# Kernel optimization log

Hardware: AMD Instinct MI355X
Metric: run time of the kernel (lower is better)

Reference implementation:

```python
import jax, jax.numpy as jnp
import numpy as np

B, Lq, D = 2, 4096, 768
NH, NP, NL = 6, 4, 1
Hs, Ws = 128, 128
Lf = Hs * Ws
DH = D // NH
EPS = 1e-6


def _ln(x, g, b):
    m = jnp.mean(x, -1, keepdims=True)
    v = jnp.mean(jnp.square(x - m), -1, keepdims=True)
    return (x - m) * jax.lax.rsqrt(v + EPS) * g + b


def setup_inputs() -> dict:
    key = jax.random.key(0)
    ks = jax.random.split(key, 20)
    s = 0.02
    rn = lambda k, shape, sc=s: (jax.random.normal(k, shape, jnp.float32) * sc)
    return {
        'query': jax.random.normal(ks[0], (B, Lq, D), jnp.float32),
        'reference_points': jax.random.uniform(ks[1], (B, Lq, NL, 2), jnp.float32),
        'feat': jax.random.normal(ks[2], (B, Lf, D), jnp.float32),
        'feat_other_modalities': jax.random.normal(ks[3], (B, Lq, D), jnp.float32),
        'spatial_shapes': jnp.array([[Hs, Ws]], jnp.int32),
        'level_start_index': jnp.array([0], jnp.int32),
        'qn_g': jnp.ones(D), 'qn_b': jnp.zeros(D),
        'fn_g': jnp.ones(D), 'fn_b': jnp.zeros(D),
        'W_off': rn(ks[4], (D, NH * NL * NP * 2)), 'b_off': jnp.zeros(NH * NL * NP * 2),
        'W_attn': rn(ks[5], (D, NH * NL * NP)), 'b_attn': jnp.zeros(NH * NL * NP),
        'W_val': rn(ks[6], (D, D)), 'b_val': jnp.zeros(D),
        'W_out': rn(ks[7], (D, D)), 'b_out': jnp.zeros(D),
        'gamma': rn(ks[8], (D,), 0.1),
        'qnm_g': jnp.ones(D), 'qnm_b': jnp.zeros(D),
        'fnm_g': jnp.ones(D), 'fnm_b': jnp.zeros(D),
        'ada_w0': rn(ks[9], (D, D // 4)), 'ada_b0': jnp.zeros(D // 4),
        'ada_w1': rn(ks[10], (D, D // 4)), 'ada_b1': jnp.zeros(D // 4),
        'ada_w2': rn(ks[11], (D // 4, D)), 'ada_b2': jnp.zeros(D),
        'gamma_om': rn(ks[12], (D,), 0.1),
    }


def _msdeform_attn(query_n, reference_points, feat_n, Hi, Wi,
                   W_off, b_off, W_attn, b_attn, W_val, b_val, W_out, b_out):
    Bv = query_n.shape[0]
    value = (feat_n @ W_val + b_val).reshape(Bv, Lf, NH, DH)
    value = value.transpose(0, 2, 1, 3)  # (B, NH, Lf, DH)

    off = (query_n @ W_off + b_off).reshape(Bv, Lq, NH, NL, NP, 2)
    aw = (query_n @ W_attn + b_attn).reshape(Bv, Lq, NH, NL * NP)
    aw = jax.nn.softmax(aw, axis=-1).reshape(Bv, Lq, NH, NL, NP)

    normalizer = jnp.array([Wi, Hi], jnp.float32)  # [W, H]
    loc = reference_points[:, :, None, :, None, :] + off / normalizer  # (B,Lq,NH,NL,NP,2)
    loc = loc[:, :, :, 0]  # single level -> (B, Lq, NH, NP, 2)

    # grid_sample align_corners=False, padding zeros
    x = loc[..., 0] * Wi - 0.5
    y = loc[..., 1] * Hi - 0.5
    x0 = jnp.floor(x); y0 = jnp.floor(y)
    wx1 = x - x0; wx0 = 1.0 - wx1
    wy1 = y - y0; wy0 = 1.0 - wy1
    x0i = x0.astype(jnp.int32); y0i = y0.astype(jnp.int32)
    x1i = x0i + 1; y1i = y0i + 1

    def t(a):  # (B,Lq,NH,NP) -> (B,NH,Lq,NP,1)
        return a.transpose(0, 2, 1, 3)[..., None]

    def gather(yy, xx):
        valid = (xx >= 0) & (xx < Wi) & (yy >= 0) & (yy < Hi)
        idx = jnp.clip(yy, 0, Hi - 1) * Wi + jnp.clip(xx, 0, Wi - 1)  # (B,Lq,NH,NP)
        idx = idx.transpose(0, 2, 1, 3).reshape(Bv, NH, Lq * NP)
        g = jnp.take_along_axis(value, idx[..., None], axis=2)  # (B,NH,Lq*NP,DH)
        g = g.reshape(Bv, NH, Lq, NP, DH)
        return g * t(valid.astype(jnp.float32))

    sampled = (gather(y0i, x0i) * t(wy0 * wx0) + gather(y0i, x1i) * t(wy0 * wx1)
               + gather(y1i, x0i) * t(wy1 * wx0) + gather(y1i, x1i) * t(wy1 * wx1))
    awT = aw[:, :, :, 0].transpose(0, 2, 1, 3)[..., None]  # (B,NH,Lq,NP,1)
    out = jnp.sum(sampled * awT, axis=3)  # (B,NH,Lq,DH)
    out = out.transpose(0, 2, 1, 3).reshape(Bv, Lq, D)
    return out @ W_out + b_out


def reference(query, reference_points, feat, feat_other_modalities, spatial_shapes,
              level_start_index, qn_g, qn_b, fn_g, fn_b, W_off, b_off, W_attn, b_attn,
              W_val, b_val, W_out, b_out, gamma, qnm_g, qnm_b, fnm_g, fnm_b,
              ada_w0, ada_b0, ada_w1, ada_b1, ada_w2, ada_b2, gamma_om):
    Hi = int(np.asarray(spatial_shapes)[0, 0]); Wi = int(np.asarray(spatial_shapes)[0, 1])
    query_n = _ln(query, qn_g, qn_b)
    feat_n = _ln(feat, fn_g, fn_b)
    attn = _msdeform_attn(query_n, reference_points, feat_n, Hi, Wi,
                          W_off, b_off, W_attn, b_attn, W_val, b_val, W_out, b_out)
    q = query + gamma * attn
    fom_n = _ln(feat_other_modalities, fnm_g, fnm_b)
    qn2 = _ln(q, qnm_g, qnm_b)
    p = qn2 @ ada_w0 + ada_b0
    xm = fom_n @ ada_w1 + ada_b1
    prompted = (p + xm) @ ada_w2 + ada_b2
    q = q + gamma_om * prompted
    return (q, prompted)
```

## Files before the change

### kernel.cpp

```cpp
#include <hip/hip_runtime.h>
#include <hip/hip_bf16.h>

typedef long long i64;

#define B_   2
#define LQ   4096
#define D_   768
#define NH_  6
#define NP_  4
#define DH_  128
#define LF   16384
#define NQ_ROWS (B_*LQ)
#define NF_ROWS (B_*LF)
#define QSIZE (NQ_ROWS*D_)

typedef __bf16 bf16x8 __attribute__((ext_vector_type(8)));
typedef float  f32x4  __attribute__((ext_vector_type(4)));

__device__ __forceinline__ float load_in(const void* p, i64 i, int bf) {
  if (bf) return __bfloat162float(((const __hip_bfloat16*)p)[i]);
  return ((const float*)p)[i];
}
__device__ __forceinline__ float us2f(unsigned short u) {
  unsigned v = (unsigned)u << 16;
  return __uint_as_float(v);
}
__device__ __forceinline__ unsigned short f2us(float f) {
  __hip_bfloat16 h = __float2bfloat16(f);
  return *(unsigned short*)&h;
}

__global__ void k_detect(const void* probe, int* flag) {
  unsigned v = *(const unsigned*)probe;
  *flag = (v == 0x3F803F80u) ? 1 : 0;
}

#define NCVT 18
struct CvtArgs { const void* src[NCVT]; float* dst[NCVT]; int n[NCVT]; };
__global__ void k_cvt(CvtArgs a, const int* flag) {
  int bf = *flag;
  int ai = blockIdx.y;
  int n = a.n[ai];
  const void* s = a.src[ai];
  float* d = a.dst[ai];
  for (int i = blockIdx.x * blockDim.x + threadIdx.x; i < n; i += gridDim.x * blockDim.x)
    d[i] = load_in(s, i, bf);
}

#define NTT 7
struct TtArgs {
  const void* src[NTT]; __hip_bfloat16* dst[NTT];
  int K[NTT]; int N[NTT]; int Nt[NTT];
  int tileBase[NTT]; int tilesN[NTT];
};
__global__ void k_transpose(TtArgs a, const int* flag) {
  __shared__ float lds[64][65];
  int bf = *flag;
  int t = blockIdx.x;
  int e = 0;
  #pragma unroll
  for (int i = 1; i < NTT; ++i) if (t >= a.tileBase[i]) e = i;
  int lt = t - a.tileBase[e];
  int tn = lt % a.tilesN[e], tk = lt / a.tilesN[e];
  int K = a.K[e], N = a.N[e], Nt = a.Nt[e];
  int k0 = tk * 64, n0 = tn * 64;
  int tid = threadIdx.x;
  int cl = tid & 63, rw = tid >> 6;
  const void* s = a.src[e];
  #pragma unroll
  for (int i = 0; i < 16; ++i) {
    int kl = rw * 16 + i;
    int n = n0 + cl;
    float v = (n < N) ? load_in(s, (i64)(k0 + kl) * N + n, bf) : 0.f;
    lds[kl][cl] = v;
  }
  __syncthreads();
  __hip_bfloat16* d = a.dst[e];
  #pragma unroll
  for (int i = 0; i < 16; ++i) {
    int nl = rw * 16 + i;
    int n = n0 + nl;
    if (n < Nt) d[(i64)n * K + k0 + cl] = __float2bfloat16(lds[cl][nl]);
  }
}

struct Ln3Args {
  const void* src0; const void* src1; const void* src2;
  const float *g0, *b0, *g1, *b1, *g2, *b2;
  __hip_bfloat16 *d0, *d1, *d2;
};
__device__ __forceinline__ void ln_row(const void* src, const float* g, const float* b,
                                       __hip_bfloat16* dst, int row, int lane, int bf) {
  float v[12];
  if (bf) {
    const ushort4* s = (const ushort4*)src + (i64)row * 192;
    #pragma unroll
    for (int j = 0; j < 3; ++j) {
      ushort4 u = s[lane + j * 64];
      v[j*4+0] = us2f(u.x); v[j*4+1] = us2f(u.y); v[j*4+2] = us2f(u.z); v[j*4+3] = us2f(u.w);
    }
  } else {
    const float4* s = (const float4*)src + (i64)row * 192;
    #pragma unroll
    for (int j = 0; j < 3; ++j) {
      float4 u = s[lane + j * 64];
      v[j*4+0] = u.x; v[j*4+1] = u.y; v[j*4+2] = u.z; v[j*4+3] = u.w;
    }
  }
  float s1 = 0.f, s2 = 0.f;
  #pragma unroll
  for (int i = 0; i < 12; ++i) { s1 += v[i]; s2 += v[i] * v[i]; }
  #pragma unroll
  for (int o = 32; o > 0; o >>= 1) { s1 += __shfl_xor(s1, o, 64); s2 += __shfl_xor(s2, o, 64); }
  float mean = s1 * (1.f / 768.f);
  float var = s2 * (1.f / 768.f) - mean * mean;
  float rstd = rsqrtf(var + 1e-6f);
  uint2* dv = (uint2*)dst + (i64)row * 192;
  #pragma unroll
  for (int j = 0; j < 3; ++j) {
    int gi = lane + j * 64;
    float4 gg = ((const float4*)g)[gi];
    float4 bb = ((const float4*)b)[gi];
    unsigned short u0 = f2us((v[j*4+0] - mean) * rstd * gg.x + bb.x);
    unsigned short u1 = f2us((v[j*4+1] - mean) * rstd * gg.y + bb.y);
    unsigned short u2 = f2us((v[j*4+2] - mean) * rstd * gg.z + bb.z);
    unsigned short u3 = f2us((v[j*4+3] - mean) * rstd * gg.w + bb.w);
    uint2 o;
    o.x = (unsigned)u0 | ((unsigned)u1 << 16);
    o.y = (unsigned)u2 | ((unsigned)u3 << 16);
    dv[gi] = o;
  }
}
__global__ void k_ln3(Ln3Args a, const int* flag) {
  int bf = *flag;
  int gw = blockIdx.x * 4 + (threadIdx.x >> 6);
  int lane = threadIdx.x & 63;
  if (gw < NF_ROWS)                 ln_row(a.src0, a.g0, a.b0, a.d0, gw,                   lane, bf);
  else if (gw < NF_ROWS + NQ_ROWS)  ln_row(a.src1, a.g1, a.b1, a.d1, gw - NF_ROWS,         lane, bf);
  else                              ln_row(a.src2, a.g2, a.b2, a.d2, gw - NF_ROWS - NQ_ROWS, lane, bf);
}
__global__ void k_ln_q(const float* src, const float* g, const float* b,
                       __hip_bfloat16* dst) {
  int gw = blockIdx.x * 4 + (threadIdx.x >> 6);
  int lane = threadIdx.x & 63;
  ln_row(src, g, b, dst, gw, lane, 0);
}

__device__ __forceinline__ void load_lds16(const void* g, void* l) {
  __builtin_amdgcn_global_load_lds((__attribute__((address_space(1))) void*)g,
                                   (__attribute__((address_space(3))) void*)l, 16, 0, 0);
}

template<int EPI>
__global__ void k_mgemm(const __hip_bfloat16* __restrict__ A, const __hip_bfloat16* __restrict__ Wt,
                        const float* __restrict__ bias, void* __restrict__ Cp,
                        int M, int N, int K, int Nx,
                        const void* aux0, const float* __restrict__ aux1, const int* flag) {
  __shared__ __align__(16) __hip_bfloat16 sm[2 * 8192];
  __hip_bfloat16* As = sm;
  __hip_bfloat16* Bs = sm + 8192;
  const int tid  = threadIdx.x;
  const int w    = tid >> 6, lane = tid & 63;
  const int quad = lane >> 4, l15 = lane & 15;
  const int f = blockIdx.x;
  const int xcd = f & 7, s8 = f >> 3;
  const int bn = (s8 % Nx) * 128;
  const int bm = (xcd + (s8 / Nx) * 8) * 128;
  const int wm = (w >> 1) * 64, wn = (w & 1) * 64;
  const int bfv = (EPI == 2 || EPI == 3) ? *flag : 0;

  int rowS[4], colS[4];
  #pragma unroll
  for (int j = 0; j < 4; ++j) {
    int p = j * 256 + tid;
    int r = p >> 3, pc = p & 7;
    rowS[j] = r; colS[j] = (pc ^ (r & 7)) * 8;
  }

  f32x4 acc[4][4];
  #pragma unroll
  for (int i = 0; i < 4; ++i)
    #pragma unroll
    for (int j = 0; j < 4; ++j) acc[i][j] = (f32x4){0.f, 0.f, 0.f, 0.f};

  const __hip_bfloat16* Ab = A  + (i64)bm * K;
  const __hip_bfloat16* Bb = Wt + (i64)bn * K;

  for (int k0 = 0; k0 < K; k0 += 64) {
    #pragma unroll
    for (int j = 0; j < 4; ++j) {
      load_lds16(Ab + (i64)rowS[j] * K + k0 + colS[j], As + (j * 256 + w * 64) * 8);
      load_lds16(Bb + (i64)rowS[j] * K + k0 + colS[j], Bs + (j * 256 + w * 64) * 8);
    }
    __syncthreads();
    bf16x8 af[2][4], bg[2][4];
    #pragma unroll
    for (int s = 0; s < 2; ++s) {
      #pragma unroll
      for (int i = 0; i < 4; ++i) {
        int ra = wm + i * 16 + l15;
        af[s][i] = *(const bf16x8*)(As + (ra * 8 + ((s * 4 + quad) ^ (ra & 7))) * 8);
        int rb = wn + i * 16 + l15;
        bg[s][i] = *(const bf16x8*)(Bs + (rb * 8 + ((s * 4 + quad) ^ (rb & 7))) * 8);
      }
    }
    #pragma unroll
    for (int s = 0; s < 2; ++s)
      #pragma unroll
      for (int i = 0; i < 4; ++i)
        #pragma unroll
        for (int j = 0; j < 4; ++j)
          acc[i][j] = __builtin_amdgcn_mfma_f32_16x16x32_bf16(af[s][i], bg[s][j], acc[i][j], 0, 0, 0);
    __syncthreads();
  }

  #pragma unroll
  for (int j = 0; j < 4; ++j) {
    int col = bn + wn + j * 16 + l15;
    if (col >= N) continue;
    float bv = bias[col];
    #pragma unroll
    for (int i = 0; i < 4; ++i) {
      #pragma unroll
      for (int r = 0; r < 4; ++r) {
        int row = bm + wm + i * 16 + quad * 4 + r;
        float v = acc[i][j][r] + bv;
        i64 idx = (i64)row * N + col;
        if (EPI == 0) {
          ((__hip_bfloat16*)Cp)[idx] = __float2bfloat16(v);
        } else if (EPI == 1) {
          ((float*)Cp)[idx] = v;
        } else if (EPI == 2) {
          ((float*)Cp)[idx] = load_in(aux0, idx, bfv) + aux1[col] * v;
        } else if (EPI == 4) {
          ((__hip_bfloat16*)Cp)[idx] = __float2bfloat16(((const float*)aux0)[idx] + v);
        } else {
          float qv = ((const float*)aux0)[idx] + aux1[col] * v;
          if (bfv) {
            ((__hip_bfloat16*)Cp)[idx]         = __float2bfloat16(qv);
            ((__hip_bfloat16*)Cp)[QSIZE + idx] = __float2bfloat16(v);
          } else {
            ((float*)Cp)[idx]         = qv;
            ((float*)Cp)[QSIZE + idx] = v;
          }
        }
      }
    }
  }
}

__global__ void k_sample(const __hip_bfloat16* __restrict__ val, const float* __restrict__ ref,
                         const float* __restrict__ oa, const int* __restrict__ ss,
                         __hip_bfloat16* __restrict__ out) {
  int gid = blockIdx.x * blockDim.x + threadIdx.x;
  int gw = gid >> 6, lane = gid & 63;
  if (gw >= B_*LQ*NH_) return;
  int h = gw % NH_;
  int bq = gw / NH_;
  int b = bq / LQ;
  int Hi = ss[0], Wi = ss[1];
  float Wf = (float)Wi, Hf = (float)Hi;
  const float* op = oa + (i64)bq*72 + h*8;
  const float* ap = oa + (i64)bq*72 + 48 + h*4;
  float rx = ref[(i64)bq*2], ry = ref[(i64)bq*2 + 1];
  float a0 = ap[0], a1 = ap[1], a2 = ap[2], a3 = ap[3];
  float mx = fmaxf(fmaxf(a0, a1), fmaxf(a2, a3));
  float e0 = expf(a0-mx), e1 = expf(a1-mx), e2 = expf(a2-mx), e3 = expf(a3-mx);
  float inv = 1.0f / (e0+e1+e2+e3);
  float wts[4] = {e0*inv, e1*inv, e2*inv, e3*inv};
  const __hip_bfloat16* vb = val + (i64)b*LF*D_ + h*DH_ + lane*2;
  float accx = 0.f, accy = 0.f;
  #pragma unroll
  for (int p = 0; p < NP_; ++p) {
    float x = rx*Wf + op[p*2+0] - 0.5f;
    float y = ry*Hf + op[p*2+1] - 0.5f;
    float xf = floorf(x), yf = floorf(y);
    int x0 = (int)xf, y0 = (int)yf;
    float wx1 = x - xf, wx0 = 1.f - wx1;
    float wy1 = y - yf, wy0 = 1.f - wy1;
    float aw = wts[p];
    #pragma unroll
    for (int c = 0; c < 4; ++c) {
      int xi = x0 + (c & 1), yi = y0 + (c >> 1);
      float wgt = aw * ((c & 1) ? wx1 : wx0) * ((c >> 1) ? wy1 : wy0);
      if (xi >= 0 && xi < Wi && yi >= 0 && yi < Hi && wgt != 0.f) {
        __hip_bfloat162 g = *(const __hip_bfloat162*)(vb + (i64)(yi*Wi + xi)*D_);
        accx += wgt * __bfloat162float(g.x); accy += wgt * __bfloat162float(g.y);
      }
    }
  }
  __hip_bfloat162 o2;
  o2.x = __float2bfloat16(accx); o2.y = __float2bfloat16(accy);
  *(__hip_bfloat162*)(out + (i64)bq*D_ + h*DH_ + lane*2) = o2;
}

extern "C" void kernel_launch(void* const* d_in, const int* in_sizes, int n_in,
                              void* d_out, int out_size, void* d_ws, size_t ws_size,
                              hipStream_t stream) {
  char* base = (char*)d_ws;
  size_t o = 0;
  auto alloc = [&](size_t bytes) { size_t r = o; o += (bytes + 63) & ~(size_t)63; return r; };
  auto F = [&](size_t off) { return (float*)(base + off); };
  auto H = [&](size_t off) { return (__hip_bfloat16*)(base + off); };

  size_t FLAG  = alloc(64);
  size_t REF   = alloc(NQ_ROWS*2*4);
  size_t QN_G  = alloc(768*4); size_t QN_B = alloc(768*4);
  size_t FN_G  = alloc(768*4); size_t FN_B = alloc(768*4);
  size_t BOA   = alloc(128*4);
  size_t BVAL  = alloc(768*4); size_t BOUT = alloc(768*4);
  size_t GAMMA = alloc(768*4);
  size_t QNM_G = alloc(768*4); size_t QNM_B = alloc(768*4);
  size_t FNM_G = alloc(768*4); size_t FNM_B = alloc(768*4);
  size_t AB0   = alloc(192*4); size_t AB1  = alloc(192*4);
  size_t AB2   = alloc(768*4); size_t GOM  = alloc(768*4);
  size_t WT_VAL = alloc((size_t)768*768*2);
  size_t WT_OUT = alloc((size_t)768*768*2);
  size_t WT_OA  = alloc((size_t)128*768*2);
  size_t WT_A0  = alloc((size_t)256*768*2);
  size_t WT_A1  = alloc((size_t)256*768*2);
  size_t WT_A2  = alloc((size_t)768*192*2);
  size_t FEATN  = alloc((size_t)NF_ROWS*768*2);
  size_t VALUE  = alloc((size_t)NF_ROWS*768*2);
  size_t QN     = alloc((size_t)NQ_ROWS*768*2);
  size_t FOMN   = alloc((size_t)NQ_ROWS*768*2);
  size_t ATTNP  = alloc((size_t)NQ_ROWS*768*2);
  size_t QN2    = alloc((size_t)NQ_ROWS*768*2);
  size_t PXM    = alloc((size_t)NQ_ROWS*192*2);
  size_t OA     = alloc((size_t)NQ_ROWS*72*4);
  size_t QBUF   = alloc((size_t)QSIZE*4);
  size_t PBUF   = alloc((size_t)NQ_ROWS*192*4);

  int* flag = (int*)(base + FLAG);

  k_detect<<<1, 1, 0, stream>>>(d_in[6], flag);

  {
    CvtArgs ca;
    const int   idx[NCVT]  = {1,6,7,8,9,11,13,15,17,18,19,20,21,22,24,26,28,29};
    const size_t dof[NCVT] = {REF,QN_G,QN_B,FN_G,FN_B,BOA,BOA+48*4,BVAL,BOUT,GAMMA,
                              QNM_G,QNM_B,FNM_G,FNM_B,AB0,AB1,AB2,GOM};
    for (int i = 0; i < NCVT; ++i) { ca.src[i] = d_in[idx[i]]; ca.dst[i] = F(dof[i]); ca.n[i] = in_sizes[idx[i]]; }
    k_cvt<<<dim3(8, NCVT), 256, 0, stream>>>(ca, flag);
  }
  {
    TtArgs ta;
    const int   src[NTT]  = {14, 16, 10, 12, 23, 25, 27};
    const size_t dst[NTT] = {WT_VAL, WT_OUT, WT_OA, WT_OA + (size_t)48*768*2, WT_A0, WT_A1, WT_A2};
    const int Kk[NTT] = {768, 768, 768, 768, 768, 768, 192};
    const int Nn[NTT] = {768, 768,  48,  24, 192, 192, 768};
    const int Nt[NTT] = {768, 768,  48,  80, 256, 256, 768};
    int tb = 0;
    for (int i = 0; i < NTT; ++i) {
      ta.src[i] = d_in[src[i]]; ta.dst[i] = H(dst[i]);
      ta.K[i] = Kk[i]; ta.N[i] = Nn[i]; ta.Nt[i] = Nt[i];
      ta.tilesN[i] = (Nt[i] + 63) / 64;
      ta.tileBase[i] = tb;
      tb += ta.tilesN[i] * (Kk[i] / 64);
    }
    k_transpose<<<tb, 256, 0, stream>>>(ta, flag);
  }

  {
    Ln3Args la;
    la.src0 = d_in[2]; la.g0 = F(FN_G);  la.b0 = F(FN_B);  la.d0 = H(FEATN);
    la.src1 = d_in[0]; la.g1 = F(QN_G);  la.b1 = F(QN_B);  la.d1 = H(QN);
    la.src2 = d_in[3]; la.g2 = F(FNM_G); la.b2 = F(FNM_B); la.d2 = H(FOMN);
    k_ln3<<<(NF_ROWS + 2*NQ_ROWS) / 4, 256, 0, stream>>>(la, flag);
  }

  k_mgemm<0><<<256*6, 256, 0, stream>>>(H(FEATN), H(WT_VAL), F(BVAL), H(VALUE),
                                        NF_ROWS, 768, 768, 6, nullptr, nullptr, flag);
  k_mgemm<1><<<64*1, 256, 0, stream>>>(H(QN), H(WT_OA), F(BOA), F(OA),
                                       NQ_ROWS, 72, 768, 1, nullptr, nullptr, flag);
  k_sample<<<(B_*LQ*NH_*64)/256, 256, 0, stream>>>(H(VALUE), F(REF), F(OA), (const int*)d_in[4], H(ATTNP));
  k_mgemm<2><<<64*6, 256, 0, stream>>>(H(ATTNP), H(WT_OUT), F(BOUT), F(QBUF),
                                       NQ_ROWS, 768, 768, 6, d_in[0], F(GAMMA), flag);
  k_ln_q<<<NQ_ROWS/4, 256, 0, stream>>>(F(QBUF), F(QNM_G), F(QNM_B), H(QN2));
  k_mgemm<1><<<64*2, 256, 0, stream>>>(H(QN2),  H(WT_A0), F(AB0), F(PBUF),
                                       NQ_ROWS, 192, 768, 2, nullptr, nullptr, flag);
  k_mgemm<4><<<64*2, 256, 0, stream>>>(H(FOMN), H(WT_A1), F(AB1), H(PXM),
                                       NQ_ROWS, 192, 768, 2, F(PBUF), nullptr, flag);
  k_mgemm<3><<<64*6, 256, 0, stream>>>(H(PXM), H(WT_A2), F(AB2), d_out,
                                       NQ_ROWS, 768, 192, 6, F(QBUF), F(GOM), flag);
}
```

Measured before the change: 531.8 us.

## Concatenate adapter GEMMs, restructure sampling per query, and drop flag kernel

```diff
diff --git a/kernel.cpp b/kernel.cpp
--- a/kernel.cpp
+++ b/kernel.cpp
@@ -17,6 +17,9 @@
 typedef __bf16 bf16x8 __attribute__((ext_vector_type(8)));
 typedef float  f32x4  __attribute__((ext_vector_type(4)));
 
+__device__ __forceinline__ int probe_bf(const void* probe) {
+  return (*(const unsigned*)probe == 0x3F803F80u) ? 1 : 0;
+}
 __device__ __forceinline__ float load_in(const void* p, i64 i, int bf) {
   if (bf) return __bfloat162float(((const __hip_bfloat16*)p)[i]);
   return ((const float*)p)[i];
@@ -30,39 +33,39 @@
   return *(unsigned short*)&h;
 }
 
-__global__ void k_detect(const void* probe, int* flag) {
-  unsigned v = *(const unsigned*)probe;
-  *flag = (v == 0x3F803F80u) ? 1 : 0;
-}
-
-#define NCVT 18
-struct CvtArgs { const void* src[NCVT]; float* dst[NCVT]; int n[NCVT]; };
-__global__ void k_cvt(CvtArgs a, const int* flag) {
-  int bf = *flag;
+#define NCVT 17
+struct CvtArgs { const void* src[NCVT]; const void* src2[NCVT]; float* dst[NCVT]; int n[NCVT]; const void* probe; };
+__global__ void k_cvt(CvtArgs a) {
+  int bf = probe_bf(a.probe);
   int ai = blockIdx.y;
   int n = a.n[ai];
   const void* s = a.src[ai];
+  const void* s2 = a.src2[ai];
   float* d = a.dst[ai];
-  for (int i = blockIdx.x * blockDim.x + threadIdx.x; i < n; i += gridDim.x * blockDim.x)
-    d[i] = load_in(s, i, bf);
+  for (int i = blockIdx.x * blockDim.x + threadIdx.x; i < n; i += gridDim.x * blockDim.x) {
+    float v = load_in(s, i, bf);
+    if (s2) v += load_in(s2, i, bf);
+    d[i] = v;
+  }
 }
 
 #define NTT 7
 struct TtArgs {
   const void* src[NTT]; __hip_bfloat16* dst[NTT];
-  int K[NTT]; int N[NTT]; int Nt[NTT];
+  int K[NTT]; int N[NTT]; int Nt[NTT]; int ds[NTT];
   int tileBase[NTT]; int tilesN[NTT];
+  const void* probe;
 };
-__global__ void k_transpose(TtArgs a, const int* flag) {
+__global__ void k_transpose(TtArgs a) {
   __shared__ float lds[64][65];
-  int bf = *flag;
+  int bf = probe_bf(a.probe);
   int t = blockIdx.x;
   int e = 0;
   #pragma unroll
   for (int i = 1; i < NTT; ++i) if (t >= a.tileBase[i]) e = i;
   int lt = t - a.tileBase[e];
   int tn = lt % a.tilesN[e], tk = lt / a.tilesN[e];
-  int K = a.K[e], N = a.N[e], Nt = a.Nt[e];
+  int K = a.K[e], N = a.N[e], Nt = a.Nt[e], ds = a.ds[e];
   int k0 = tk * 64, n0 = tn * 64;
   int tid = threadIdx.x;
   int cl = tid & 63, rw = tid >> 6;
@@ -80,7 +83,64 @@
   for (int i = 0; i < 16; ++i) {
     int nl = rw * 16 + i;
     int n = n0 + nl;
-    if (n < Nt) d[(i64)n * K + k0 + cl] = __float2bfloat16(lds[cl][nl]);
+    if (n < Nt) d[(i64)n * ds + k0 + cl] = __float2bfloat16(lds[cl][nl]);
+  }
+}
+
+__device__ __forceinline__ void ln_row32(const void* src, i64 so, const float* g, const float* b,
+                                         __hip_bfloat16* dst, i64 dofs, int sl, int bf) {
+  float v[24];
+  if (bf) {
+    const unsigned short* s = (const unsigned short*)src + so;
+    #pragma unroll
+    for (int j = 0; j < 3; ++j) {
+      uint4 u = *(const uint4*)(s + (i64)(j * 32 + sl) * 8);
+      v[j*8+0] = us2f((unsigned short)u.x); v[j*8+1] = us2f((unsigned short)(u.x >> 16));
+      v[j*8+2] = us2f((unsigned short)u.y); v[j*8+3] = us2f((unsigned short)(u.y >> 16));
+      v[j*8+4] = us2f((unsigned short)u.z); v[j*8+5] = us2f((unsigned short)(u.z >> 16));
+      v[j*8+6] = us2f((unsigned short)u.w); v[j*8+7] = us2f((unsigned short)(u.w >> 16));
+    }
+  } else {
+    const float* s = (const float*)src + so;
+    #pragma unroll
+    for (int j = 0; j < 6; ++j) {
+      float4 u = *(const float4*)(s + (i64)(j * 32 + sl) * 4);
+      v[j*4+0] = u.x; v[j*4+1] = u.y; v[j*4+2] = u.z; v[j*4+3] = u.w;
+    }
+  }
+  float s1 = 0.f, s2 = 0.f;
+  #pragma unroll
+  for (int i = 0; i < 24; ++i) { s1 += v[i]; s2 += v[i] * v[i]; }
+  #pragma unroll
+  for (int o = 16; o > 0; o >>= 1) { s1 += __shfl_xor(s1, o, 64); s2 += __shfl_xor(s2, o, 64); }
+  float mean = s1 * (1.f / 768.f);
+  float var = s2 * (1.f / 768.f) - mean * mean;
+  float rstd = rsqrtf(var + 1e-6f);
+  unsigned short* dp = (unsigned short*)dst + dofs;
+  if (bf) {
+    #pragma unroll
+    for (int j = 0; j < 3; ++j) {
+      int gi = (j * 32 + sl) * 8;
+      float4 g0 = *(const float4*)(g + gi), g1 = *(const float4*)(g + gi + 4);
+      float4 b0 = *(const float4*)(b + gi), b1 = *(const float4*)(b + gi + 4);
+      uint4 o;
+      o.x = (unsigned)f2us((v[j*8+0]-mean)*rstd*g0.x+b0.x) | ((unsigned)f2us((v[j*8+1]-mean)*rstd*g0.y+b0.y) << 16);
+      o.y = (unsigned)f2us((v[j*8+2]-mean)*rstd*g0.z+b0.z) | ((unsigned)f2us((v[j*8+3]-mean)*rstd*g0.w+b0.w) << 16);
+      o.z = (unsigned)f2us((v[j*8+4]-mean)*rstd*g1.x+b1.x) | ((unsigned)f2us((v[j*8+5]-mean)*rstd*g1.y+b1.y) << 16);
+      o.w = (unsigned)f2us((v[j*8+6]-mean)*rstd*g1.z+b1.z) | ((unsigned)f2us((v[j*8+7]-mean)*rstd*g1.w+b1.w) << 16);
+      *(uint4*)(dp + gi) = o;
+    }
+  } else {
+    #pragma unroll
+    for (int j = 0; j < 6; ++j) {
+      int gi = (j * 32 + sl) * 4;
+      float4 g0 = *(const float4*)(g + gi);
+      float4 b0 = *(const float4*)(b + gi);
+      uint2 o;
+      o.x = (unsigned)f2us((v[j*4+0]-mean)*rstd*g0.x+b0.x) | ((unsigned)f2us((v[j*4+1]-mean)*rstd*g0.y+b0.y) << 16);
+      o.y = (unsigned)f2us((v[j*4+2]-mean)*rstd*g0.z+b0.z) | ((unsigned)f2us((v[j*4+3]-mean)*rstd*g0.w+b0.w) << 16);
+      *(uint2*)(dp + gi) = o;
+    }
   }
 }
 
@@ -88,62 +148,26 @@
   const void* src0; const void* src1; const void* src2;
   const float *g0, *b0, *g1, *b1, *g2, *b2;
   __hip_bfloat16 *d0, *d1, *d2;
+  const void* probe;
 };
-__device__ __forceinline__ void ln_row(const void* src, const float* g, const float* b,
-                                       __hip_bfloat16* dst, int row, int lane, int bf) {
-  float v[12];
-  if (bf) {
-    const ushort4* s = (const ushort4*)src + (i64)row * 192;
-    #pragma unroll
-    for (int j = 0; j < 3; ++j) {
-      ushort4 u = s[lane + j * 64];
-      v[j*4+0] = us2f(u.x); v[j*4+1] = us2f(u.y); v[j*4+2] = us2f(u.z); v[j*4+3] = us2f(u.w);
-    }
+__global__ void k_ln3(Ln3Args a) {
+  int bf = probe_bf(a.probe);
+  int row = blockIdx.x * 8 + (threadIdx.x >> 5);
+  int sl = threadIdx.x & 31;
+  if (row < NF_ROWS) {
+    ln_row32(a.src0, (i64)row * 768, a.g0, a.b0, a.d0, (i64)row * 768, sl, bf);
+  } else if (row < NF_ROWS + NQ_ROWS) {
+    int r = row - NF_ROWS;
+    ln_row32(a.src1, (i64)r * 768, a.g1, a.b1, a.d1, (i64)r * 768, sl, bf);
   } else {
-    const float4* s = (const float4*)src + (i64)row * 192;
-    #pragma unroll
-    for (int j = 0; j < 3; ++j) {
-      float4 u = s[lane + j * 64];
-      v[j*4+0] = u.x; v[j*4+1] = u.y; v[j*4+2] = u.z; v[j*4+3] = u.w;
-    }
-  }
-  float s1 = 0.f, s2 = 0.f;
-  #pragma unroll
-  for (int i = 0; i < 12; ++i) { s1 += v[i]; s2 += v[i] * v[i]; }
-  #pragma unroll
-  for (int o = 32; o > 0; o >>= 1) { s1 += __shfl_xor(s1, o, 64); s2 += __shfl_xor(s2, o, 64); }
-  float mean = s1 * (1.f / 768.f);
-  float var = s2 * (1.f / 768.f) - mean * mean;
-  float rstd = rsqrtf(var + 1e-6f);
-  uint2* dv = (uint2*)dst + (i64)row * 192;
-  #pragma unroll
-  for (int j = 0; j < 3; ++j) {
-    int gi = lane + j * 64;
-    float4 gg = ((const float4*)g)[gi];
-    float4 bb = ((const float4*)b)[gi];
-    unsigned short u0 = f2us((v[j*4+0] - mean) * rstd * gg.x + bb.x);
-    unsigned short u1 = f2us((v[j*4+1] - mean) * rstd * gg.y + bb.y);
-    unsigned short u2 = f2us((v[j*4+2] - mean) * rstd * gg.z + bb.z);
-    unsigned short u3 = f2us((v[j*4+3] - mean) * rstd * gg.w + bb.w);
-    uint2 o;
-    o.x = (unsigned)u0 | ((unsigned)u1 << 16);
-    o.y = (unsigned)u2 | ((unsigned)u3 << 16);
-    dv[gi] = o;
-  }
-}
-__global__ void k_ln3(Ln3Args a, const int* flag) {
-  int bf = *flag;
-  int gw = blockIdx.x * 4 + (threadIdx.x >> 6);
-  int lane = threadIdx.x & 63;
-  if (gw < NF_ROWS)                 ln_row(a.src0, a.g0, a.b0, a.d0, gw,                   lane, bf);
-  else if (gw < NF_ROWS + NQ_ROWS)  ln_row(a.src1, a.g1, a.b1, a.d1, gw - NF_ROWS,         lane, bf);
-  else                              ln_row(a.src2, a.g2, a.b2, a.d2, gw - NF_ROWS - NQ_ROWS, lane, bf);
-}
-__global__ void k_ln_q(const float* src, const float* g, const float* b,
-                       __hip_bfloat16* dst) {
-  int gw = blockIdx.x * 4 + (threadIdx.x >> 6);
-  int lane = threadIdx.x & 63;
-  ln_row(src, g, b, dst, gw, lane, 0);
+    int r = row - NF_ROWS - NQ_ROWS;
+    ln_row32(a.src2, (i64)r * 768, a.g2, a.b2, a.d2, (i64)r * 1536 + 768, sl, bf);
+  }
+}
+__global__ void k_ln_q(const float* src, const float* g, const float* b, __hip_bfloat16* dst) {
+  int row = blockIdx.x * 8 + (threadIdx.x >> 5);
+  int sl = threadIdx.x & 31;
+  ln_row32(src, (i64)row * 768, g, b, dst, (i64)row * 1536, sl, 0);
 }
 
 __device__ __forceinline__ void load_lds16(const void* g, void* l) {
@@ -155,7 +179,7 @@
 __global__ void k_mgemm(const __hip_bfloat16* __restrict__ A, const __hip_bfloat16* __restrict__ Wt,
                         const float* __restrict__ bias, void* __restrict__ Cp,
                         int M, int N, int K, int Nx,
-                        const void* aux0, const float* __restrict__ aux1, const int* flag) {
+                        const void* aux0, const float* __restrict__ aux1, const void* probe) {
   __shared__ __align__(16) __hip_bfloat16 sm[2 * 8192];
   __hip_bfloat16* As = sm;
   __hip_bfloat16* Bs = sm + 8192;
@@ -167,7 +191,7 @@
   const int bn = (s8 % Nx) * 128;
   const int bm = (xcd + (s8 / Nx) * 8) * 128;
   const int wm = (w >> 1) * 64, wn = (w & 1) * 64;
-  const int bfv = (EPI == 2 || EPI == 3) ? *flag : 0;
+  const int bfv = (EPI == 2 || EPI == 3) ? probe_bf(probe) : 0;
 
   int rowS[4], colS[4];
   #pragma unroll
@@ -232,8 +256,6 @@
           ((float*)Cp)[idx] = v;
         } else if (EPI == 2) {
           ((float*)Cp)[idx] = load_in(aux0, idx, bfv) + aux1[col] * v;
-        } else if (EPI == 4) {
-          ((__hip_bfloat16*)Cp)[idx] = __float2bfloat16(((const float*)aux0)[idx] + v);
         } else {
           float qv = ((const float*)aux0)[idx] + aux1[col] * v;
           if (bfv) {
@@ -252,46 +274,58 @@
 __global__ void k_sample(const __hip_bfloat16* __restrict__ val, const float* __restrict__ ref,
                          const float* __restrict__ oa, const int* __restrict__ ss,
                          __hip_bfloat16* __restrict__ out) {
-  int gid = blockIdx.x * blockDim.x + threadIdx.x;
-  int gw = gid >> 6, lane = gid & 63;
-  if (gw >= B_*LQ*NH_) return;
-  int h = gw % NH_;
-  int bq = gw / NH_;
-  int b = bq / LQ;
+  int gw = blockIdx.x * 4 + (threadIdx.x >> 6);
+  if (gw >= NQ_ROWS) return;
+  int lane = threadIdx.x & 63;
+  int sg = lane >> 4, sl = lane & 15;
+  int bq = gw, b = bq >> 12;
   int Hi = ss[0], Wi = ss[1];
   float Wf = (float)Wi, Hf = (float)Hi;
-  const float* op = oa + (i64)bq*72 + h*8;
-  const float* ap = oa + (i64)bq*72 + 48 + h*4;
   float rx = ref[(i64)bq*2], ry = ref[(i64)bq*2 + 1];
-  float a0 = ap[0], a1 = ap[1], a2 = ap[2], a3 = ap[3];
-  float mx = fmaxf(fmaxf(a0, a1), fmaxf(a2, a3));
-  float e0 = expf(a0-mx), e1 = expf(a1-mx), e2 = expf(a2-mx), e3 = expf(a3-mx);
-  float inv = 1.0f / (e0+e1+e2+e3);
-  float wts[4] = {e0*inv, e1*inv, e2*inv, e3*inv};
-  const __hip_bfloat16* vb = val + (i64)b*LF*D_ + h*DH_ + lane*2;
-  float accx = 0.f, accy = 0.f;
-  #pragma unroll
-  for (int p = 0; p < NP_; ++p) {
-    float x = rx*Wf + op[p*2+0] - 0.5f;
-    float y = ry*Hf + op[p*2+1] - 0.5f;
-    float xf = floorf(x), yf = floorf(y);
-    int x0 = (int)xf, y0 = (int)yf;
-    float wx1 = x - xf, wx0 = 1.f - wx1;
-    float wy1 = y - yf, wy0 = 1.f - wy1;
-    float aw = wts[p];
-    #pragma unroll
-    for (int c = 0; c < 4; ++c) {
-      int xi = x0 + (c & 1), yi = y0 + (c >> 1);
-      float wgt = aw * ((c & 1) ? wx1 : wx0) * ((c >> 1) ? wy1 : wy0);
-      if (xi >= 0 && xi < Wi && yi >= 0 && yi < Hi && wgt != 0.f) {
-        __hip_bfloat162 g = *(const __hip_bfloat162*)(vb + (i64)(yi*Wi + xi)*D_);
-        accx += wgt * __bfloat162float(g.x); accy += wgt * __bfloat162float(g.y);
+  const float* orow = oa + (i64)bq * 72;
+  const __hip_bfloat16* vb = val + (i64)b * LF * D_;
+  int cx = sg & 1, cy = sg >> 1;
+  #pragma unroll
+  for (int h = 0; h < NH_; ++h) {
+    const float* ap = orow + 48 + h*4;
+    float a0 = ap[0], a1 = ap[1], a2 = ap[2], a3 = ap[3];
+    float mx = fmaxf(fmaxf(a0, a1), fmaxf(a2, a3));
+    float e0 = __expf(a0-mx), e1 = __expf(a1-mx), e2 = __expf(a2-mx), e3 = __expf(a3-mx);
+    float inv = 1.0f / (e0+e1+e2+e3);
+    float wts[4] = {e0*inv, e1*inv, e2*inv, e3*inv};
+    const float* op = orow + h*8;
+    float acc[8];
+    #pragma unroll
+    for (int e = 0; e < 8; ++e) acc[e] = 0.f;
+    #pragma unroll
+    for (int p = 0; p < NP_; ++p) {
+      float x = rx*Wf + op[p*2+0] - 0.5f;
+      float y = ry*Hf + op[p*2+1] - 0.5f;
+      float xf = floorf(x), yf = floorf(y);
+      int x0 = (int)xf, y0 = (int)yf;
+      float wx1 = x - xf, wy1 = y - yf;
+      int xi = x0 + cx, yi = y0 + cy;
+      float wgt = wts[p] * (cx ? wx1 : 1.f - wx1) * (cy ? wy1 : 1.f - wy1);
+      if (xi >= 0 && xi < Wi && yi >= 0 && yi < Hi) {
+        bf16x8 g = *(const bf16x8*)(vb + (i64)(yi*Wi + xi)*D_ + h*DH_ + sl*8);
+        #pragma unroll
+        for (int e = 0; e < 8; ++e) acc[e] += wgt * (float)g[e];
       }
     }
-  }
-  __hip_bfloat162 o2;
-  o2.x = __float2bfloat16(accx); o2.y = __float2bfloat16(accy);
-  *(__hip_bfloat162*)(out + (i64)bq*D_ + h*DH_ + lane*2) = o2;
+    #pragma unroll
+    for (int e = 0; e < 8; ++e) {
+      acc[e] += __shfl_xor(acc[e], 16, 64);
+      acc[e] += __shfl_xor(acc[e], 32, 64);
+    }
+    if (sg == 0) {
+      uint4 o;
+      o.x = (unsigned)f2us(acc[0]) | ((unsigned)f2us(acc[1]) << 16);
+      o.y = (unsigned)f2us(acc[2]) | ((unsigned)f2us(acc[3]) << 16);
+      o.z = (unsigned)f2us(acc[4]) | ((unsigned)f2us(acc[5]) << 16);
+      o.w = (unsigned)f2us(acc[6]) | ((unsigned)f2us(acc[7]) << 16);
+      *(uint4*)(out + (i64)bq*D_ + h*DH_ + sl*8) = o;
+    }
+  }
 }
 
 extern "C" void kernel_launch(void* const* d_in, const int* in_sizes, int n_in,
@@ -302,8 +336,8 @@
   auto alloc = [&](size_t bytes) { size_t r = o; o += (bytes + 63) & ~(size_t)63; return r; };
   auto F = [&](size_t off) { return (float*)(base + off); };
   auto H = [&](size_t off) { return (__hip_bfloat16*)(base + off); };
-
-  size_t FLAG  = alloc(64);
+  const void* probe = d_in[6];
+
   size_t REF   = alloc(NQ_ROWS*2*4);
   size_t QN_G  = alloc(768*4); size_t QN_B = alloc(768*4);
   size_t FN_G  = alloc(768*4); size_t FN_B = alloc(768*4);
@@ -312,75 +346,75 @@
   size_t GAMMA = alloc(768*4);
   size_t QNM_G = alloc(768*4); size_t QNM_B = alloc(768*4);
   size_t FNM_G = alloc(768*4); size_t FNM_B = alloc(768*4);
-  size_t AB0   = alloc(192*4); size_t AB1  = alloc(192*4);
+  size_t AB01  = alloc(192*4);
   size_t AB2   = alloc(768*4); size_t GOM  = alloc(768*4);
   size_t WT_VAL = alloc((size_t)768*768*2);
   size_t WT_OUT = alloc((size_t)768*768*2);
   size_t WT_OA  = alloc((size_t)128*768*2);
-  size_t WT_A0  = alloc((size_t)256*768*2);
-  size_t WT_A1  = alloc((size_t)256*768*2);
+  size_t WT_A01 = alloc((size_t)256*1536*2);
   size_t WT_A2  = alloc((size_t)768*192*2);
   size_t FEATN  = alloc((size_t)NF_ROWS*768*2);
   size_t VALUE  = alloc((size_t)NF_ROWS*768*2);
   size_t QN     = alloc((size_t)NQ_ROWS*768*2);
-  size_t FOMN   = alloc((size_t)NQ_ROWS*768*2);
+  size_t QNF    = alloc((size_t)NQ_ROWS*1536*2);
   size_t ATTNP  = alloc((size_t)NQ_ROWS*768*2);
-  size_t QN2    = alloc((size_t)NQ_ROWS*768*2);
   size_t PXM    = alloc((size_t)NQ_ROWS*192*2);
   size_t OA     = alloc((size_t)NQ_ROWS*72*4);
   size_t QBUF   = alloc((size_t)QSIZE*4);
-  size_t PBUF   = alloc((size_t)NQ_ROWS*192*4);
-
-  int* flag = (int*)(base + FLAG);
-
-  k_detect<<<1, 1, 0, stream>>>(d_in[6], flag);
 
   {
     CvtArgs ca;
-    const int   idx[NCVT]  = {1,6,7,8,9,11,13,15,17,18,19,20,21,22,24,26,28,29};
+    const int   idx[NCVT]  = {1,6,7,8,9,11,13,15,17,18,19,20,21,22,24,28,29};
     const size_t dof[NCVT] = {REF,QN_G,QN_B,FN_G,FN_B,BOA,BOA+48*4,BVAL,BOUT,GAMMA,
-                              QNM_G,QNM_B,FNM_G,FNM_B,AB0,AB1,AB2,GOM};
-    for (int i = 0; i < NCVT; ++i) { ca.src[i] = d_in[idx[i]]; ca.dst[i] = F(dof[i]); ca.n[i] = in_sizes[idx[i]]; }
-    k_cvt<<<dim3(8, NCVT), 256, 0, stream>>>(ca, flag);
+                              QNM_G,QNM_B,FNM_G,FNM_B,AB01,AB2,GOM};
+    for (int i = 0; i < NCVT; ++i) {
+      ca.src[i] = d_in[idx[i]]; ca.src2[i] = nullptr;
+      ca.dst[i] = F(dof[i]); ca.n[i] = in_sizes[idx[i]];
+    }
+    ca.src2[14] = d_in[26];
+    ca.probe = probe;
+    k_cvt<<<dim3(8, NCVT), 256, 0, stream>>>(ca);
   }
   {
     TtArgs ta;
     const int   src[NTT]  = {14, 16, 10, 12, 23, 25, 27};
-    const size_t dst[NTT] = {WT_VAL, WT_OUT, WT_OA, WT_OA + (size_t)48*768*2, WT_A0, WT_A1, WT_A2};
-    const int Kk[NTT] = {768, 768, 768, 768, 768, 768, 192};
-    const int Nn[NTT] = {768, 768,  48,  24, 192, 192, 768};
-    const int Nt[NTT] = {768, 768,  48,  80, 256, 256, 768};
+    const size_t dst[NTT] = {WT_VAL, WT_OUT, WT_OA, WT_OA + (size_t)48*768*2,
+                             WT_A01, WT_A01 + (size_t)768*2, WT_A2};
+    const int Kk[NTT] = {768, 768, 768, 768, 768,  768, 192};
+    const int Nn[NTT] = {768, 768,  48,  24, 192,  192, 768};
+    const int Nt[NTT] = {768, 768,  48,  80, 256,  256, 768};
+    const int Ds[NTT] = {768, 768, 768, 768, 1536, 1536, 192};
     int tb = 0;
     for (int i = 0; i < NTT; ++i) {
       ta.src[i] = d_in[src[i]]; ta.dst[i] = H(dst[i]);
-      ta.K[i] = Kk[i]; ta.N[i] = Nn[i]; ta.Nt[i] = Nt[i];
+      ta.K[i] = Kk[i]; ta.N[i] = Nn[i]; ta.Nt[i] = Nt[i]; ta.ds[i] = Ds[i];
       ta.tilesN[i] = (Nt[i] + 63) / 64;
       ta.tileBase[i] = tb;
       tb += ta.tilesN[i] * (Kk[i] / 64);
     }
-    k_transpose<<<tb, 256, 0, stream>>>(ta, flag);
+    ta.probe = probe;
+    k_transpose<<<tb, 256, 0, stream>>>(ta);
   }
 
   {
     Ln3Args la;
     la.src0 = d_in[2]; la.g0 = F(FN_G);  la.b0 = F(FN_B);  la.d0 = H(FEATN);
     la.src1 = d_in[0]; la.g1 = F(QN_G);  la.b1 = F(QN_B);  la.d1 = H(QN);
-    la.src2 = d_in[3]; la.g2 = F(FNM_G); la.b2 = F(FNM_B); la.d2 = H(FOMN);
-    k_ln3<<<(NF_ROWS + 2*NQ_ROWS) / 4, 256, 0, stream>>>(la, flag);
+    la.src2 = d_in[3]; la.g2 = F(FNM_G); la.b2 = F(FNM_B); la.d2 = H(QNF);
+    la.probe = probe;
+    k_ln3<<<(NF_ROWS + 2*NQ_ROWS) / 8, 256, 0, stream>>>(la);
   }
 
   k_mgemm<0><<<256*6, 256, 0, stream>>>(H(FEATN), H(WT_VAL), F(BVAL), H(VALUE),
-                                        NF_ROWS, 768, 768, 6, nullptr, nullptr, flag);
+                                        NF_ROWS, 768, 768, 6, nullptr, nullptr, probe);
   k_mgemm<1><<<64*1, 256, 0, stream>>>(H(QN), H(WT_OA), F(BOA), F(OA),
-                                       NQ_ROWS, 72, 768, 1, nullptr, nullptr, flag);
-  k_sample<<<(B_*LQ*NH_*64)/256, 256, 0, stream>>>(H(VALUE), F(REF), F(OA), (const int*)d_in[4], H(ATTNP));
+                                       NQ_ROWS, 72, 768, 1, nullptr, nullptr, probe);
+  k_sample<<<NQ_ROWS/4, 256, 0, stream>>>(H(VALUE), F(REF), F(OA), (const int*)d_in[4], H(ATTNP));
   k_mgemm<2><<<64*6, 256, 0, stream>>>(H(ATTNP), H(WT_OUT), F(BOUT), F(QBUF),
-                                       NQ_ROWS, 768, 768, 6, d_in[0], F(GAMMA), flag);
-  k_ln_q<<<NQ_ROWS/4, 256, 0, stream>>>(F(QBUF), F(QNM_G), F(QNM_B), H(QN2));
-  k_mgemm<1><<<64*2, 256, 0, stream>>>(H(QN2),  H(WT_A0), F(AB0), F(PBUF),
-                                       NQ_ROWS, 192, 768, 2, nullptr, nullptr, flag);
-  k_mgemm<4><<<64*2, 256, 0, stream>>>(H(FOMN), H(WT_A1), F(AB1), H(PXM),
-                                       NQ_ROWS, 192, 768, 2, F(PBUF), nullptr, flag);
+                                       NQ_ROWS, 768, 768, 6, d_in[0], F(GAMMA), probe);
+  k_ln_q<<<NQ_ROWS/8, 256, 0, stream>>>(F(QBUF), F(QNM_G), F(QNM_B), H(QNF));
+  k_mgemm<0><<<64*2, 256, 0, stream>>>(H(QNF), H(WT_A01), F(AB01), H(PXM),
+                                       NQ_ROWS, 192, 1536, 2, nullptr, nullptr, probe);
   k_mgemm<3><<<64*6, 256, 0, stream>>>(H(PXM), H(WT_A2), F(AB2), d_out,
-                                       NQ_ROWS, 768, 192, 6, F(QBUF), F(GOM), flag);
-}
+                                       NQ_ROWS, 768, 192, 6, F(QBUF), F(GOM), probe);
+}
```

Measured after the change: 483.2 us. 1.1x faster.
